# Kernel optimization log

Measured on AMD Instinct MI355X. Metric: run time of the kernel, lower is better.

## Reference

```python
import jax, jax.numpy as jnp
import numpy as np

N_NODES = 50000
N_EDGES = 800000
F_IN = 128
F_OUT = 128
DROP_RATE = 0.6  # torch F.dropout(p=0.6, training=True default)


def setup_inputs() -> dict:
    key = jax.random.key(0)
    k1, k2, k3, k4, k5, k6 = jax.random.split(key, 6)
    x = jax.random.normal(k1, (N_NODES, F_IN), dtype=jnp.float32)
    # edge list: src = center node (sorted, mimics per-node neighbor-list grouping), dst = neighbor
    src = jnp.sort(jax.random.randint(k2, (N_EDGES,), 0, N_NODES, dtype=jnp.int64))
    dst = jax.random.randint(k3, (N_EDGES,), 0, N_NODES, dtype=jnp.int64)
    adj_vals = jax.random.uniform(k4, (N_EDGES,), dtype=jnp.float32)  # normalized adj weights
    stdv = 1.0 / np.sqrt(F_OUT)
    w_mask = jax.random.normal(k5, (2 * F_IN, F_IN), dtype=jnp.float32) * stdv
    w0 = jax.random.uniform(k6, (F_IN, F_OUT), minval=-stdv, maxval=stdv, dtype=jnp.float32)
    return {"x": x, "src": src, "dst": dst, "adj_vals": adj_vals, "w_mask": w_mask, "w0": w0}


def reference(x, src, dst, adj_vals, w_mask, w0):
    # Edge-wise gather of center and neighbor features: [E, F] each
    cen = x[src]
    nei = x[dst]
    # Per-edge mask: sigmoid(concat(center, neighbor) @ W_mask)  -> [E, F]
    m = jax.nn.sigmoid(jnp.concatenate([cen, nei], axis=1) @ w_mask)
    # Dropout p=0.6 (deterministic key for reproducibility), torch-style inverted scaling
    keep = jax.random.bernoulli(jax.random.key(42), 1.0 - DROP_RATE, m.shape)
    m = jnp.where(keep, m / (1.0 - DROP_RATE), jnp.zeros_like(m))
    # Masked weighted neighbor sum per center node, plus the center feature itself
    agg = jax.ops.segment_sum(m * nei, src, num_segments=N_NODES)
    x_new = x + agg
    # Dense projection, then spmm(adj, support) over the same edge structure
    support = x_new @ w0
    out = jax.ops.segment_sum(adj_vals[:, None] * support[dst], src, num_segments=N_NODES)
    return out
```

## Files before the change

### kernel.cpp

```cpp
#include <hip/hip_runtime.h>
#include <stdint.h>


#define THREEFRY_PARTITIONABLE 1

#define NNODES 50000
#define FDIM 128

__device__ __forceinline__ uint32_t rotl32(uint32_t x, int r) {
  return (x << r) | (x >> (32 - r));
}

__device__ __forceinline__ void threefry2x32(uint32_t k0, uint32_t k1,
                                             uint32_t x0, uint32_t x1,
                                             uint32_t& o0, uint32_t& o1) {
  uint32_t k2 = k0 ^ k1 ^ 0x1BD11BDAu;
  x0 += k0; x1 += k1;
  x0 += x1; x1 = rotl32(x1, 13); x1 ^= x0;
  x0 += x1; x1 = rotl32(x1, 15); x1 ^= x0;
  x0 += x1; x1 = rotl32(x1, 26); x1 ^= x0;
  x0 += x1; x1 = rotl32(x1,  6); x1 ^= x0;
  x0 += k1; x1 += k2 + 1u;
  x0 += x1; x1 = rotl32(x1, 17); x1 ^= x0;
  x0 += x1; x1 = rotl32(x1, 29); x1 ^= x0;
  x0 += x1; x1 = rotl32(x1, 16); x1 ^= x0;
  x0 += x1; x1 = rotl32(x1, 24); x1 ^= x0;
  x0 += k2; x1 += k0 + 2u;
  x0 += x1; x1 = rotl32(x1, 13); x1 ^= x0;
  x0 += x1; x1 = rotl32(x1, 15); x1 ^= x0;
  x0 += x1; x1 = rotl32(x1, 26); x1 ^= x0;
  x0 += x1; x1 = rotl32(x1,  6); x1 ^= x0;
  x0 += k0; x1 += k1 + 3u;
  x0 += x1; x1 = rotl32(x1, 17); x1 ^= x0;
  x0 += x1; x1 = rotl32(x1, 29); x1 ^= x0;
  x0 += x1; x1 = rotl32(x1, 16); x1 ^= x0;
  x0 += x1; x1 = rotl32(x1, 24); x1 ^= x0;
  x0 += k1; x1 += k2 + 4u;
  x0 += x1; x1 = rotl32(x1, 13); x1 ^= x0;
  x0 += x1; x1 = rotl32(x1, 15); x1 ^= x0;
  x0 += x1; x1 = rotl32(x1, 26); x1 ^= x0;
  x0 += x1; x1 = rotl32(x1,  6); x1 ^= x0;
  x0 += k2; x1 += k0 + 5u;
  o0 = x0; o1 = x1;
}

__device__ __forceinline__ bool keep_drop(uint32_t idx, uint32_t total) {
#if THREEFRY_PARTITIONABLE
  uint32_t o0, o1;
  threefry2x32(0u, 42u, 0u, idx, o0, o1);
  uint32_t bits = o0 ^ o1;
#else
  uint32_t H = total >> 1;
  uint32_t j = (idx < H) ? idx : (idx - H);
  uint32_t o0, o1;
  threefry2x32(0u, 42u, j, j + H, o0, o1);
  uint32_t bits = (idx < H) ? o0 : o1;
#endif
  float u = __uint_as_float((bits >> 9) | 0x3f800000u) - 1.0f;
  return u < 0.4000000059604645f;
}

__device__ __forceinline__ bool detect_i64(const int* p, int n) {
  int i = (n / 2) | 1;
  return p[i] == 0 && p[i + 2] == 0 && p[i + 4] == 0;
}

__device__ __forceinline__ int idx_at(const void* p, int i, bool is64) {
  return is64 ? (int)((const long long*)p)[i] : ((const int*)p)[i];
}

__device__ __forceinline__ int lower_bound_idx(const void* a, int n, bool is64, int v) {
  int lo = 0, hi = n;
  while (lo < hi) {
    int mid = (lo + hi) >> 1;
    if (idx_at(a, mid, is64) < v) lo = mid + 1; else hi = mid;
  }
  return lo;
}

__global__ __launch_bounds__(256) void rowptr_kernel(const void* __restrict__ src, int nE,
                                                     int* __restrict__ rowptr) {
  bool is64 = detect_i64((const int*)src, nE);
  int n = blockIdx.x * blockDim.x + threadIdx.x;
  if (n <= NNODES) rowptr[n] = lower_bound_idx(src, nE, is64, n);
}

#define MM_ROWS 8
__global__ __launch_bounds__(128) void matmul128(const float* __restrict__ in,
                                                 const float* __restrict__ W,
                                                 float* __restrict__ out, int nrows) {
  __shared__ float xs[MM_ROWS][FDIM];
  int r0 = blockIdx.x * MM_ROWS;
  int t = threadIdx.x;
  #pragma unroll
  for (int r = 0; r < MM_ROWS; ++r) {
    int row = r0 + r;
    xs[r][t] = (row < nrows) ? in[row * FDIM + t] : 0.0f;
  }
  __syncthreads();
  float acc[MM_ROWS] = {};
  #pragma unroll 4
  for (int k = 0; k < FDIM; ++k) {
    float w = W[k * FDIM + t];
    #pragma unroll
    for (int r = 0; r < MM_ROWS; ++r) acc[r] += xs[r][k] * w;
  }
  #pragma unroll
  for (int r = 0; r < MM_ROWS; ++r) {
    int row = r0 + r;
    if (row < nrows) out[row * FDIM + t] = acc[r];
  }
}

__global__ __launch_bounds__(128) void edge_agg(const float* __restrict__ x,
                                                const void* __restrict__ dst,
                                                const int* __restrict__ rowptr,
                                                const float* __restrict__ A,
                                                const float* __restrict__ B,
                                                float* __restrict__ x_new, int nE) {
  bool is64 = detect_i64((const int*)dst, nE);
  int n = blockIdx.x;
  int f = threadIdx.x;
  int lo = rowptr[n], hi = rowptr[n + 1];
  float a = A[n * FDIM + f];
  float acc = 0.0f;
  uint32_t total = (uint32_t)nE * (uint32_t)FDIM;
  for (int e = lo; e < hi; ++e) {
    int d = idx_at(dst, e, is64);
    d = min(max(d, 0), NNODES - 1);
    float z = a + B[d * FDIM + f];
    float m = 1.0f / (1.0f + expf(-z));
    uint32_t idx = (uint32_t)e * (uint32_t)FDIM + (uint32_t)f;
    if (keep_drop(idx, total)) acc += (m * 2.5f) * x[d * FDIM + f];
  }
  x_new[n * FDIM + f] = x[n * FDIM + f] + acc;
}

__global__ __launch_bounds__(128) void edge_out(const float* __restrict__ support,
                                                const void* __restrict__ dst,
                                                const int* __restrict__ rowptr,
                                                const float* __restrict__ adj,
                                                float* __restrict__ out, int nE) {
  bool is64 = detect_i64((const int*)dst, nE);
  int n = blockIdx.x;
  int f = threadIdx.x;
  int lo = rowptr[n], hi = rowptr[n + 1];
  float acc = 0.0f;
  for (int e = lo; e < hi; ++e) {
    int d = idx_at(dst, e, is64);
    d = min(max(d, 0), NNODES - 1);
    acc += adj[e] * support[d * FDIM + f];
  }
  out[n * FDIM + f] = acc;
}

extern "C" void kernel_launch(void* const* d_in, const int* in_sizes, int n_in,
                              void* d_out, int out_size, void* d_ws, size_t ws_size,
                              hipStream_t stream) {
  const float* x      = (const float*)d_in[0];
  const void*  src    = d_in[1];
  const void*  dst    = d_in[2];
  const float* adj    = (const float*)d_in[3];
  const float* w_mask = (const float*)d_in[4];
  const float* w0     = (const float*)d_in[5];
  float* out = (float*)d_out;

  int nE = in_sizes[1];
  const size_t NF = (size_t)NNODES * FDIM;

  float* A       = (float*)d_ws;
  float* B       = A + NF;
  float* x_new   = B + NF;
  int*   rowptr  = (int*)(x_new + NF);
  float* support = A;

  rowptr_kernel<<<(NNODES + 256) / 256, 256, 0, stream>>>(src, nE, rowptr);
  matmul128<<<(NNODES + MM_ROWS - 1) / MM_ROWS, 128, 0, stream>>>(x, w_mask, A, NNODES);
  matmul128<<<(NNODES + MM_ROWS - 1) / MM_ROWS, 128, 0, stream>>>(x, w_mask + FDIM * FDIM, B, NNODES);
  edge_agg<<<NNODES, 128, 0, stream>>>(x, dst, rowptr, A, B, x_new, nE);
  matmul128<<<(NNODES + MM_ROWS - 1) / MM_ROWS, 128, 0, stream>>>(x_new, w0, support, NNODES);
  edge_out<<<NNODES, 128, 0, stream>>>(support, dst, rowptr, adj, out, nE);
}
```

Measured before the change: 569.9 us.

## Fuse mask matmuls, precompute int32 dst, unroll edge loops, use fast sigmoid

Merges the two w_mask matmuls into one kernel so the x tile is loaded once and produces both halves. Grows the row tile to 16 with float4 shared-memory reads. Adds a kernel that converts dst to clamped int32 once, so the edge kernels skip int64 detection and clamping. The edge loops are unrolled by four with independent accumulators to raise memory-level parallelism. The dropout test becomes an integer threshold compare and sigmoid uses hardware exp2/rcp, which may differ slightly in rounding from the reference.

```diff
diff --git a/kernel.cpp b/kernel.cpp
--- a/kernel.cpp
+++ b/kernel.cpp
@@ -1,8 +1,6 @@
 #include <hip/hip_runtime.h>
 #include <stdint.h>
 
-
-#define THREEFRY_PARTITIONABLE 1
 
 #define NNODES 50000
 #define FDIM 128
@@ -44,20 +42,15 @@
   o0 = x0; o1 = x1;
 }
 
-__device__ __forceinline__ bool keep_drop(uint32_t idx, uint32_t total) {
-#if THREEFRY_PARTITIONABLE
+__device__ __forceinline__ bool keep_drop(uint32_t idx) {
   uint32_t o0, o1;
   threefry2x32(0u, 42u, 0u, idx, o0, o1);
-  uint32_t bits = o0 ^ o1;
-#else
-  uint32_t H = total >> 1;
-  uint32_t j = (idx < H) ? idx : (idx - H);
-  uint32_t o0, o1;
-  threefry2x32(0u, 42u, j, j + H, o0, o1);
-  uint32_t bits = (idx < H) ? o0 : o1;
-#endif
-  float u = __uint_as_float((bits >> 9) | 0x3f800000u) - 1.0f;
-  return u < 0.4000000059604645f;
+  return (o0 ^ o1) < 1717987328u;
+}
+
+__device__ __forceinline__ float sigmoid_f(float z) {
+  float e = __builtin_amdgcn_exp2f(z * -1.44269504088896340736f);
+  return __builtin_amdgcn_rcpf(1.0f + e);
 }
 
 __device__ __forceinline__ bool detect_i64(const int* p, int n) {
@@ -85,73 +78,144 @@
   if (n <= NNODES) rowptr[n] = lower_bound_idx(src, nE, is64, n);
 }
 
-#define MM_ROWS 8
-__global__ __launch_bounds__(128) void matmul128(const float* __restrict__ in,
-                                                 const float* __restrict__ W,
-                                                 float* __restrict__ out, int nrows) {
-  __shared__ float xs[MM_ROWS][FDIM];
-  int r0 = blockIdx.x * MM_ROWS;
+__global__ __launch_bounds__(256) void cvt_dst(const void* __restrict__ dst, int nE,
+                                               int* __restrict__ dst32) {
+  bool is64 = detect_i64((const int*)dst, nE);
+  int i = blockIdx.x * blockDim.x + threadIdx.x;
+  if (i < nE) {
+    int d = idx_at(dst, i, is64);
+    dst32[i] = min(max(d, 0), NNODES - 1);
+  }
+}
+
+#define MMR 16
+__global__ __launch_bounds__(128) void matmulAB(const float* __restrict__ in,
+                                                const float* __restrict__ W,
+                                                float* __restrict__ A,
+                                                float* __restrict__ B, int nrows) {
+  __shared__ float xs[MMR][FDIM];
+  int r0 = blockIdx.x * MMR;
   int t = threadIdx.x;
   #pragma unroll
-  for (int r = 0; r < MM_ROWS; ++r) {
+  for (int r = 0; r < MMR; ++r) {
     int row = r0 + r;
     xs[r][t] = (row < nrows) ? in[row * FDIM + t] : 0.0f;
   }
   __syncthreads();
-  float acc[MM_ROWS] = {};
-  #pragma unroll 4
-  for (int k = 0; k < FDIM; ++k) {
-    float w = W[k * FDIM + t];
+  float accA[MMR] = {}, accB[MMR] = {};
+  for (int k = 0; k < FDIM; k += 4) {
+    float wa0 = W[(k + 0) * FDIM + t], wa1 = W[(k + 1) * FDIM + t];
+    float wa2 = W[(k + 2) * FDIM + t], wa3 = W[(k + 3) * FDIM + t];
+    float wb0 = W[(FDIM + k + 0) * FDIM + t], wb1 = W[(FDIM + k + 1) * FDIM + t];
+    float wb2 = W[(FDIM + k + 2) * FDIM + t], wb3 = W[(FDIM + k + 3) * FDIM + t];
     #pragma unroll
-    for (int r = 0; r < MM_ROWS; ++r) acc[r] += xs[r][k] * w;
-  }
-  #pragma unroll
-  for (int r = 0; r < MM_ROWS; ++r) {
+    for (int r = 0; r < MMR; ++r) {
+      float4 xv = *(const float4*)&xs[r][k];
+      accA[r] += xv.x * wa0; accA[r] += xv.y * wa1;
+      accA[r] += xv.z * wa2; accA[r] += xv.w * wa3;
+      accB[r] += xv.x * wb0; accB[r] += xv.y * wb1;
+      accB[r] += xv.z * wb2; accB[r] += xv.w * wb3;
+    }
+  }
+  #pragma unroll
+  for (int r = 0; r < MMR; ++r) {
+    int row = r0 + r;
+    if (row < nrows) { A[row * FDIM + t] = accA[r]; B[row * FDIM + t] = accB[r]; }
+  }
+}
+
+__global__ __launch_bounds__(128) void matmul16(const float* __restrict__ in,
+                                                const float* __restrict__ W,
+                                                float* __restrict__ out, int nrows) {
+  __shared__ float xs[MMR][FDIM];
+  int r0 = blockIdx.x * MMR;
+  int t = threadIdx.x;
+  #pragma unroll
+  for (int r = 0; r < MMR; ++r) {
+    int row = r0 + r;
+    xs[r][t] = (row < nrows) ? in[row * FDIM + t] : 0.0f;
+  }
+  __syncthreads();
+  float acc[MMR] = {};
+  for (int k = 0; k < FDIM; k += 4) {
+    float w0 = W[(k + 0) * FDIM + t], w1 = W[(k + 1) * FDIM + t];
+    float w2 = W[(k + 2) * FDIM + t], w3 = W[(k + 3) * FDIM + t];
+    #pragma unroll
+    for (int r = 0; r < MMR; ++r) {
+      float4 xv = *(const float4*)&xs[r][k];
+      acc[r] += xv.x * w0; acc[r] += xv.y * w1;
+      acc[r] += xv.z * w2; acc[r] += xv.w * w3;
+    }
+  }
+  #pragma unroll
+  for (int r = 0; r < MMR; ++r) {
     int row = r0 + r;
     if (row < nrows) out[row * FDIM + t] = acc[r];
   }
 }
 
 __global__ __launch_bounds__(128) void edge_agg(const float* __restrict__ x,
-                                                const void* __restrict__ dst,
+                                                const int* __restrict__ dst32,
                                                 const int* __restrict__ rowptr,
                                                 const float* __restrict__ A,
                                                 const float* __restrict__ B,
-                                                float* __restrict__ x_new, int nE) {
-  bool is64 = detect_i64((const int*)dst, nE);
+                                                float* __restrict__ x_new) {
   int n = blockIdx.x;
   int f = threadIdx.x;
   int lo = rowptr[n], hi = rowptr[n + 1];
-  float a = A[n * FDIM + f];
-  float acc = 0.0f;
-  uint32_t total = (uint32_t)nE * (uint32_t)FDIM;
-  for (int e = lo; e < hi; ++e) {
-    int d = idx_at(dst, e, is64);
-    d = min(max(d, 0), NNODES - 1);
-    float z = a + B[d * FDIM + f];
-    float m = 1.0f / (1.0f + expf(-z));
-    uint32_t idx = (uint32_t)e * (uint32_t)FDIM + (uint32_t)f;
-    if (keep_drop(idx, total)) acc += (m * 2.5f) * x[d * FDIM + f];
-  }
-  x_new[n * FDIM + f] = x[n * FDIM + f] + acc;
+  const float* Bf = B + f;
+  const float* xf = x + f;
+  float a = A[(n << 7) + f];
+  float acc0 = 0.f, acc1 = 0.f, acc2 = 0.f, acc3 = 0.f;
+  uint32_t idx = ((uint32_t)lo << 7) + (uint32_t)f;
+  int e = lo;
+  for (; e + 4 <= hi; e += 4, idx += 512u) {
+    int d0 = dst32[e + 0], d1 = dst32[e + 1], d2 = dst32[e + 2], d3 = dst32[e + 3];
+    float b0 = Bf[d0 << 7], xv0 = xf[d0 << 7];
+    float b1 = Bf[d1 << 7], xv1 = xf[d1 << 7];
+    float b2 = Bf[d2 << 7], xv2 = xf[d2 << 7];
+    float b3 = Bf[d3 << 7], xv3 = xf[d3 << 7];
+    bool k0 = keep_drop(idx);
+    bool k1 = keep_drop(idx + 128u);
+    bool k2 = keep_drop(idx + 256u);
+    bool k3 = keep_drop(idx + 384u);
+    float m0 = sigmoid_f(a + b0), m1 = sigmoid_f(a + b1);
+    float m2 = sigmoid_f(a + b2), m3 = sigmoid_f(a + b3);
+    acc0 += k0 ? (m0 * 2.5f) * xv0 : 0.0f;
+    acc1 += k1 ? (m1 * 2.5f) * xv1 : 0.0f;
+    acc2 += k2 ? (m2 * 2.5f) * xv2 : 0.0f;
+    acc3 += k3 ? (m3 * 2.5f) * xv3 : 0.0f;
+  }
+  for (; e < hi; ++e, idx += 128u) {
+    int d = dst32[e];
+    float m = sigmoid_f(a + Bf[d << 7]);
+    if (keep_drop(idx)) acc0 += (m * 2.5f) * xf[d << 7];
+  }
+  float acc = (acc0 + acc1) + (acc2 + acc3);
+  x_new[(n << 7) + f] = x[(n << 7) + f] + acc;
 }
 
 __global__ __launch_bounds__(128) void edge_out(const float* __restrict__ support,
-                                                const void* __restrict__ dst,
+                                                const int* __restrict__ dst32,
                                                 const int* __restrict__ rowptr,
                                                 const float* __restrict__ adj,
-                                                float* __restrict__ out, int nE) {
-  bool is64 = detect_i64((const int*)dst, nE);
+                                                float* __restrict__ out) {
   int n = blockIdx.x;
   int f = threadIdx.x;
   int lo = rowptr[n], hi = rowptr[n + 1];
-  float acc = 0.0f;
-  for (int e = lo; e < hi; ++e) {
-    int d = idx_at(dst, e, is64);
-    d = min(max(d, 0), NNODES - 1);
-    acc += adj[e] * support[d * FDIM + f];
-  }
-  out[n * FDIM + f] = acc;
+  const float* Sf = support + f;
+  float a0 = 0.f, a1 = 0.f, a2 = 0.f, a3 = 0.f;
+  int e = lo;
+  for (; e + 4 <= hi; e += 4) {
+    int d0 = dst32[e + 0], d1 = dst32[e + 1], d2 = dst32[e + 2], d3 = dst32[e + 3];
+    float w0 = adj[e + 0], w1 = adj[e + 1], w2 = adj[e + 2], w3 = adj[e + 3];
+    a0 += w0 * Sf[d0 << 7];
+    a1 += w1 * Sf[d1 << 7];
+    a2 += w2 * Sf[d2 << 7];
+    a3 += w3 * Sf[d3 << 7];
+  }
+  for (; e < hi; ++e) a0 += adj[e] * Sf[dst32[e] << 7];
+  out[(n << 7) + f] = (a0 + a1) + (a2 + a3);
 }
 
 extern "C" void kernel_launch(void* const* d_in, const int* in_sizes, int n_in,
@@ -172,12 +236,13 @@
   float* B       = A + NF;
   float* x_new   = B + NF;
   int*   rowptr  = (int*)(x_new + NF);
+  int*   dst32   = rowptr + (NNODES + 1);
   float* support = A;
 
   rowptr_kernel<<<(NNODES + 256) / 256, 256, 0, stream>>>(src, nE, rowptr);
-  matmul128<<<(NNODES + MM_ROWS - 1) / MM_ROWS, 128, 0, stream>>>(x, w_mask, A, NNODES);
-  matmul128<<<(NNODES + MM_ROWS - 1) / MM_ROWS, 128, 0, stream>>>(x, w_mask + FDIM * FDIM, B, NNODES);
-  edge_agg<<<NNODES, 128, 0, stream>>>(x, dst, rowptr, A, B, x_new, nE);
-  matmul128<<<(NNODES + MM_ROWS - 1) / MM_ROWS, 128, 0, stream>>>(x_new, w0, support, NNODES);
-  edge_out<<<NNODES, 128, 0, stream>>>(support, dst, rowptr, adj, out, nE);
-}
+  cvt_dst<<<(nE + 255) / 256, 256, 0, stream>>>(dst, nE, dst32);
+  matmulAB<<<(NNODES + MMR - 1) / MMR, 128, 0, stream>>>(x, w_mask, A, B, NNODES);
+  edge_agg<<<NNODES, 128, 0, stream>>>(x, dst32, rowptr, A, B, x_new);
+  matmul16<<<(NNODES + MMR - 1) / MMR, 128, 0, stream>>>(x_new, w0, support, NNODES);
+  edge_out<<<NNODES, 128, 0, stream>>>(support, dst32, rowptr, adj, out);
+}
```

Result: faster. 505.0 us (-11.4%).
